# Kernel optimization log

Measured on AMD Instinct MI355X. Metric: run time of the kernel, lower is better.

## Reference

```python
import jax, jax.numpy as jnp
import numpy as np

N_NODES = 50000
N_EDGES = 800000
DIM = 64


def _param(key, shape, scale):
    return jax.random.normal(key, shape, dtype=jnp.float32) * scale


def setup_inputs() -> dict:
    key = jax.random.key(0)
    ks = jax.random.split(key, 20)
    s = 1.0 / np.sqrt(DIM)
    x = jax.random.normal(ks[0], (N_NODES, DIM), dtype=jnp.float32)
    weights = jax.random.uniform(ks[1], (6,), dtype=jnp.float32)
    edge_index = jax.random.randint(ks[2], (2, N_EDGES), 0, N_NODES, dtype=jnp.int64)
    return {
        "x": x,
        "weights": weights,
        # mlp
        "W_mlp": _param(ks[3], (DIM, DIM), s), "b_mlp": jnp.zeros((DIM,), jnp.float32),
        # sage (mean aggregator): lin_l on neighbor mean, lin_r on self
        "Wl_sage": _param(ks[4], (DIM, DIM), s), "Wr_sage": _param(ks[5], (DIM, DIM), s),
        "b_sage": jnp.zeros((DIM,), jnp.float32),
        # gcn
        "W_gcn": _param(ks[6], (DIM, DIM), s), "b_gcn": jnp.zeros((DIM,), jnp.float32),
        # gat (single head)
        "W_gat": _param(ks[7], (DIM, DIM), s),
        "a_src": _param(ks[8], (DIM,), s), "a_dst": _param(ks[9], (DIM,), s),
        "b_gat": jnp.zeros((DIM,), jnp.float32),
        # chebconv K=3
        "W_cheb": _param(ks[10], (3, DIM, DIM), s), "b_cheb": jnp.zeros((DIM,), jnp.float32),
        # gin (eps=0, nn = Linear)
        "W_gin": _param(ks[11], (DIM, DIM), s), "b_gin": jnp.zeros((DIM,), jnp.float32),
        "edge_index": edge_index,
    }


def _mixed_forward(x, weights, W_mlp, b_mlp, Wl_sage, Wr_sage, b_sage,
                   W_gcn, b_gcn, W_gat, a_src, a_dst, b_gat,
                   W_cheb, b_cheb, W_gin, b_gin, edge_index):
    N = x.shape[0]
    src, dst = edge_index[0], edge_index[1]
    seg_sum = lambda v, idx: jax.ops.segment_sum(v, idx, num_segments=N)

    deg = seg_sum(jnp.ones(src.shape[0], x.dtype), dst)  # in-degree [N]
    nsum = seg_sum(x[src], dst)                           # sum of neighbor feats [N, D]

    # --- mlp (graph-free) ---
    o_mlp = x @ W_mlp + b_mlp

    # --- sage, mean aggregation ---
    nmean = nsum / jnp.maximum(deg, 1.0)[:, None]
    o_sage = nmean @ Wl_sage + x @ Wr_sage + b_sage

    # --- gcn with self loops: D'^{-1/2} (A+I) D'^{-1/2} X W ---
    dinv = jax.lax.rsqrt(deg + 1.0)
    xw = x @ W_gcn
    norm_e = dinv[src] * dinv[dst]
    o_gcn = seg_sum(norm_e[:, None] * xw[src], dst) + xw * (dinv * dinv)[:, None] + b_gcn

    # --- gat, single head, self loops appended, leaky_relu(0.2) scoring ---
    h = x @ W_gat
    el, er = h @ a_src, h @ a_dst
    loop = jnp.arange(N, dtype=src.dtype)
    src2 = jnp.concatenate([src, loop])
    dst2 = jnp.concatenate([dst, loop])
    e = jax.nn.leaky_relu(el[src2] + er[dst2], 0.2)
    m = jax.ops.segment_max(e, dst2, num_segments=N)
    p = jnp.exp(e - m[dst2])
    z = jax.ops.segment_sum(p, dst2, num_segments=N)
    alpha = p / (z[dst2] + 1e-16)
    o_gat = jax.ops.segment_sum(alpha[:, None] * h[src2], dst2, num_segments=N) + b_gat

    # --- cheb K=3, lambda_max=2: L_hat = L_norm - I = -A_norm ---
    dinv_c = jax.lax.rsqrt(jnp.maximum(deg, 1.0))
    nrm = dinv_c[src] * dinv_c[dst]
    prop = lambda t: seg_sum(nrm[:, None] * t[src], dst)
    T0 = x
    T1 = -prop(T0)
    T2 = -2.0 * prop(T1) - T0
    o_cheb = T0 @ W_cheb[0] + T1 @ W_cheb[1] + T2 @ W_cheb[2] + b_cheb

    # --- gin, eps=0, nn = Linear ---
    o_gin = (x + nsum) @ W_gin + b_gin

    outs = (o_mlp, o_sage, o_gcn, o_gat, o_cheb, o_gin)
    res = jnp.zeros_like(o_mlp)
    for k, o in enumerate(outs):
        res = res + weights[k] * jax.nn.elu(o)
    return res


def reference(x, weights, W_mlp, b_mlp, Wl_sage, Wr_sage, b_sage,
              W_gcn, b_gcn, W_gat, a_src, a_dst, b_gat,
              W_cheb, b_cheb, W_gin, b_gin, edge_index):
    return _mixed_forward(x, weights, W_mlp, b_mlp, Wl_sage, Wr_sage, b_sage,
                          W_gcn, b_gcn, W_gat, a_src, a_dst, b_gat,
                          W_cheb, b_cheb, W_gin, b_gin, edge_index)
```

## Files before the change

### kernel.cpp

```cpp
#include <hip/hip_runtime.h>
#include <cstdint>
#include <cstddef>

#define NN 50000
#define NE 800000
#define CAP 96

constexpr size_t O_CNT   = 0;
constexpr size_t O_SLOT  = 50048;
constexpr size_t O_NODAL = O_SLOT + (size_t)NN*CAP;
constexpr size_t O_VA    = O_NODAL + 200000;
constexpr size_t O_VB    = O_VA + 64;
constexpr size_t O_XB    = O_VB + 64;
constexpr size_t O_NSB   = O_XB + 1600032;
constexpr size_t O_T1B   = O_NSB + 1600000;
constexpr size_t O_V1B   = O_T1B + 1600032;
constexpr size_t O_GB    = O_V1B + 1600000;
constexpr size_t O_UB    = O_GB  + 1600000;
constexpr size_t O_WPK   = O_UB  + 1600000;

typedef __attribute__((ext_vector_type(8))) short short8;
typedef __attribute__((ext_vector_type(4))) float f32x4;

__device__ __forceinline__ float leaky02(float v){ return v >= 0.f ? v : 0.2f*v; }
__device__ __forceinline__ float eluf(float v){ return v > 0.f ? v : (__expf(v) - 1.f); }

__device__ __forceinline__ void lds_fence(){
  asm volatile("s_waitcnt lgkmcnt(0)" ::: "memory");
}

__device__ __forceinline__ unsigned short f2bf(float f){
  unsigned u = __float_as_uint(f);
  unsigned r = (u + 0x7FFFu + ((u >> 16) & 1u)) >> 16;
  return (unsigned short)r;
}
__device__ __forceinline__ float bf2f(unsigned short b){
  return __uint_as_float(((unsigned)b) << 16);
}

__global__ void k_scatter(const int4* __restrict__ src4, const int4* __restrict__ dst4,
                          int* __restrict__ cnt, int* __restrict__ slot){
  int i = blockIdx.x*256 + threadIdx.x;
  if (i >= NE/4) return;
  int4 s = src4[i], d = dst4[i];
  int pos;
  pos = atomicAdd(&cnt[d.x], 1); if (pos < CAP) slot[(size_t)d.x*CAP + pos] = s.x;
  pos = atomicAdd(&cnt[d.y], 1); if (pos < CAP) slot[(size_t)d.y*CAP + pos] = s.y;
  pos = atomicAdd(&cnt[d.z], 1); if (pos < CAP) slot[(size_t)d.z*CAP + pos] = s.z;
  pos = atomicAdd(&cnt[d.w], 1); if (pos < CAP) slot[(size_t)d.w*CAP + pos] = s.w;
}

__global__ void k_xcast(const float4* __restrict__ x4, ushort4* __restrict__ xb4,
                        ushort4* __restrict__ t1b4){
  int i = blockIdx.x*256 + threadIdx.x;
  if (i < NN*16){
    float4 v = x4[i];
    ushort4 o;
    o.x = f2bf(v.x); o.y = f2bf(v.y); o.z = f2bf(v.z); o.w = f2bf(v.w);
    xb4[i] = o;
  } else if (i < (NN+1)*16){
    ushort4 z; z.x = 0; z.y = 0; z.z = 0; z.w = 0;
    xb4[i] = z;
    t1b4[i] = z;
  }
}

__global__ void k_va(const float* __restrict__ Wg, const float* __restrict__ a_src,
                     const float* __restrict__ a_dst, float* __restrict__ va, float* __restrict__ vb){
  int k = threadIdx.x;
  float sa = 0.f, sb = 0.f;
  for (int j = 0; j < 64; ++j){
    float w = Wg[k*64 + j];
    sa = fmaf(w, a_src[j], sa);
    sb = fmaf(w, a_dst[j], sb);
  }
  va[k] = sa; vb[k] = sb;
}

__global__ void k_wprep(const float* __restrict__ W_mlp, const float* __restrict__ Wr,
                        const float* __restrict__ W_cheb, const float* __restrict__ W_gin,
                        const float* __restrict__ Wl, const float* __restrict__ W_gcn,
                        const float* __restrict__ W_gat, unsigned short* __restrict__ wpk){
  int w = blockIdx.x;
  const float* s; const float* sub = nullptr;
  switch (w){
    case 0: s = W_mlp; break;
    case 1: s = Wr; break;
    case 2: s = W_cheb; sub = W_cheb + 8192; break;
    case 3: s = W_gin; break;
    case 4: s = Wl; break;
    case 5: s = W_cheb + 4096; break;
    case 6: s = W_cheb + 8192; break;
    case 7: s = W_gcn; break;
    default: s = W_gat; break;
  }
  for (int e = threadIdx.x; e < 4096; e += 256){
    int k = e >> 6, n = e & 63;
    float f = s[e];
    if (sub) f -= sub[e];
    wpk[(size_t)w*4096 + (size_t)n*64 + k] = f2bf(f);
  }
}

__global__ __launch_bounds__(256) void k_nodal(const float* __restrict__ x,
    const int* __restrict__ cnt, const float* __restrict__ va, const float* __restrict__ vb,
    float4* __restrict__ nodal){
  int tid = threadIdx.x;
  int li = tid & 15;
  int row = blockIdx.x*16 + (tid >> 4);
  if (row >= NN) return;
  float4 hv = *(const float4*)&x[(size_t)row*64 + li*4];
  float4 av = *(const float4*)&va[li*4];
  float4 bv = *(const float4*)&vb[li*4];
  float ps = hv.x*av.x + hv.y*av.y + hv.z*av.z + hv.w*av.w;
  float pd = hv.x*bv.x + hv.y*bv.y + hv.z*bv.z + hv.w*bv.w;
  #pragma unroll
  for (int o = 1; o < 16; o <<= 1){ ps += __shfl_xor(ps, o); pd += __shfl_xor(pd, o); }
  if (li == 0){
    float c = (float)cnt[row];
    float dinv  = rsqrtf(c + 1.f);
    float dinvc = rsqrtf(fmaxf(c, 1.f));
    nodal[row] = make_float4(dinvc, dinv, ps, pd);
  }
}

__global__ __launch_bounds__(256) void k_aggA(const float* __restrict__ x,
    const unsigned short* __restrict__ xb,
    const int* __restrict__ cnt, const int* __restrict__ slot,
    const float4* __restrict__ nodal,
    unsigned short* __restrict__ nsb, unsigned short* __restrict__ t1b,
    unsigned short* __restrict__ v1b, unsigned short* __restrict__ gb){
  __shared__ float4 sW[4][64];
  int wid  = threadIdx.x >> 6;
  int lane = threadIdx.x & 63;
  int node = blockIdx.x*4 + wid;
  if (node >= NN) return;
  int c = min(cnt[node], CAP);
  const int* sl = slot + (size_t)node*CAP;
  float4 nn = nodal[node];
  float ern = nn.w;
  float a0 = 0.f, a1 = 0.f, a2 = 0.f, a3 = 0.f, zl = 0.f;
  for (int base = 0; base < c; base += 64){
    int rem = min(64, c - base);
    bool act = lane < rem;
    int s = act ? sl[base+lane] : NN;
    float4 ns = act ? nodal[s] : make_float4(0.f,0.f,0.f,0.f);
    float p = act ? __expf(fminf(leaky02(ns.z + ern), 60.f)) : 0.f;
    zl += p;
    sW[wid][lane] = make_float4(__int_as_float(s), ns.x, ns.y, p);
    lds_fence();
    for (int j = 0; j < rem; j += 8){
      float4 w[8];
      #pragma unroll
      for (int jj = 0; jj < 8; ++jj) w[jj] = sW[wid][j + jj];
      float vv[8];
      #pragma unroll
      for (int jj = 0; jj < 8; ++jj){
        int sb = __float_as_int(w[jj].x);
        sb = ((unsigned)sb <= (unsigned)NN) ? sb : NN;
        vv[jj] = bf2f(xb[(size_t)sb*64 + lane]);
      }
      #pragma unroll
      for (int jj = 0; jj < 8; ++jj){
        a0 += vv[jj];
        a1 = fmaf(w[jj].y, vv[jj], a1);
        a2 = fmaf(w[jj].z, vv[jj], a2);
        a3 = fmaf(w[jj].w, vv[jj], a3);
      }
    }
    lds_fence();
  }
  #pragma unroll
  for (int o = 32; o > 0; o >>= 1) zl += __shfl_xor(zl, o);
  float xs = x[(size_t)node*64 + lane];
  float p_self = __expf(fminf(leaky02(nn.z + nn.w), 60.f));
  float rz = 1.f / (zl + p_self + 1e-16f);
  size_t off = (size_t)node*64 + lane;
  nsb[off] = f2bf(a0);
  t1b[off] = f2bf(-nn.x * a1);
  v1b[off] = f2bf(nn.y*a2 + nn.y*nn.y*xs);
  gb[off]  = f2bf((a3 + p_self*xs) * rz);
}

__global__ __launch_bounds__(256) void k_aggB(const unsigned short* __restrict__ t1b,
    const int* __restrict__ cnt, const int* __restrict__ slot,
    const float4* __restrict__ nodal, unsigned short* __restrict__ ub){
  __shared__ float2 sW[4][64];
  int wid  = threadIdx.x >> 6;
  int lane = threadIdx.x & 63;
  int node = blockIdx.x*4 + wid;
  if (node >= NN) return;
  int c = min(cnt[node], CAP);
  const int* sl = slot + (size_t)node*CAP;
  const float* nf = (const float*)nodal;
  float acc = 0.f;
  for (int base = 0; base < c; base += 64){
    int rem = min(64, c - base);
    bool act = lane < rem;
    int s = act ? sl[base+lane] : NN;
    float dc = act ? nf[(size_t)s*4] : 0.f;
    sW[wid][lane] = make_float2(__int_as_float(s), dc);
    lds_fence();
    for (int j = 0; j < rem; j += 8){
      float2 w[8];
      #pragma unroll
      for (int jj = 0; jj < 8; ++jj) w[jj] = sW[wid][j + jj];
      float tv[8];
      #pragma unroll
      for (int jj = 0; jj < 8; ++jj){
        int sb = __float_as_int(w[jj].x);
        sb = ((unsigned)sb <= (unsigned)NN) ? sb : NN;
        tv[jj] = bf2f(t1b[(size_t)sb*64 + lane]);
      }
      #pragma unroll
      for (int jj = 0; jj < 8; ++jj)
        acc = fmaf(w[jj].y, tv[jj], acc);
    }
    lds_fence();
  }
  ub[(size_t)node*64 + lane] = f2bf(-2.f * nodal[node].x * acc);
}

__global__ __launch_bounds__(64) void k_epi(
    const float* __restrict__ wts,
    const float* __restrict__ b_mlp, const float* __restrict__ b_sage,
    const float* __restrict__ b_gcn, const float* __restrict__ b_gat,
    const float* __restrict__ b_cheb, const float* __restrict__ b_gin,
    const float4* __restrict__ nodal, const unsigned short* __restrict__ wpk,
    const unsigned short* __restrict__ xb, const unsigned short* __restrict__ nsb,
    const unsigned short* __restrict__ t1b, const unsigned short* __restrict__ v1b,
    const unsigned short* __restrict__ gb, const unsigned short* __restrict__ ub,
    float* __restrict__ out){
  const int lane = threadIdx.x;
  const int ml   = lane & 15;
  const int q    = lane >> 4;
  const int rowbase = blockIdx.x*16;
  const float w0 = wts[0], w1 = wts[1], w2 = wts[2], w3 = wts[3], w4 = wts[4], w5 = wts[5];
  const float* nod = (const float*)nodal;

  short8 ah0, ah1;

  auto loadA = [&](const unsigned short* __restrict__ src){
    const unsigned short* p = src + (size_t)(rowbase + ml)*64 + q*8;
    ah0 = *(const short8*)p;
    ah1 = *(const short8*)(p + 32);
  };
  auto group = [&](int w, f32x4 acc[4]){
    const unsigned short* base = wpk + (size_t)w*4096;
    #pragma unroll
    for (int nt = 0; nt < 4; ++nt){
      const unsigned short* bp = base + (size_t)(nt*16 + ml)*64;
      short8 b0 = *(const short8*)(bp + q*8);
      short8 b1 = *(const short8*)(bp + 32 + q*8);
      acc[nt] = __builtin_amdgcn_mfma_f32_16x16x32_bf16(ah0, b0, acc[nt], 0, 0, 0);
      acc[nt] = __builtin_amdgcn_mfma_f32_16x16x32_bf16(ah1, b1, acc[nt], 0, 0, 0);
    }
  };

  f32x4 res[4];
  #pragma unroll
  for (int i = 0; i < 4; ++i) res[i] = (f32x4){0.f,0.f,0.f,0.f};

  auto emit = [&](const f32x4 acc[4], const float* __restrict__ bias, float wk){
    #pragma unroll
    for (int nt = 0; nt < 4; ++nt){
      float b = bias[nt*16 + ml];
      #pragma unroll
      for (int r = 0; r < 4; ++r) res[nt][r] += wk * eluf(acc[nt][r] + b);
    }
  };

  f32x4 t[4], accC[4], accWr[4], accG[4];

  loadA(v1b);
  #pragma unroll
  for (int i=0;i<4;++i) t[i] = (f32x4){0.f,0.f,0.f,0.f};
  group(7, t); emit(t, b_gcn, w2);
  loadA(gb);
  #pragma unroll
  for (int i=0;i<4;++i) t[i] = (f32x4){0.f,0.f,0.f,0.f};
  group(8, t); emit(t, b_gat, w3);
  loadA(ub);
  #pragma unroll
  for (int i=0;i<4;++i) accC[i] = (f32x4){0.f,0.f,0.f,0.f};
  group(6, accC);
  loadA(t1b);
  group(5, accC);
  loadA(xb);
  #pragma unroll
  for (int i=0;i<4;++i) t[i] = (f32x4){0.f,0.f,0.f,0.f};
  group(0, t); emit(t, b_mlp, w0);
  #pragma unroll
  for (int i=0;i<4;++i) accWr[i] = (f32x4){0.f,0.f,0.f,0.f};
  group(1, accWr);
  group(2, accC); emit(accC, b_cheb, w4);
  #pragma unroll
  for (int i=0;i<4;++i) accG[i] = (f32x4){0.f,0.f,0.f,0.f};
  group(3, accG);
  loadA(nsb);
  group(3, accG); emit(accG, b_gin, w5);
  #pragma unroll
  for (int i=0;i<4;++i) t[i] = (f32x4){0.f,0.f,0.f,0.f};
  group(4, t);
  #pragma unroll
  for (int nt = 0; nt < 4; ++nt){
    float b = b_sage[nt*16 + ml];
    #pragma unroll
    for (int r = 0; r < 4; ++r){
      int row = rowbase + q*4 + r;
      float dc = nod[(size_t)row*4];
      float invd = dc*dc;
      res[nt][r] += w1 * eluf(invd*t[nt][r] + accWr[nt][r] + b);
    }
  }
  #pragma unroll
  for (int nt = 0; nt < 4; ++nt){
    int col = nt*16 + ml;
    #pragma unroll
    for (int r = 0; r < 4; ++r){
      int row = rowbase + q*4 + r;
      out[(size_t)row*64 + col] = res[nt][r];
    }
  }
}

extern "C" void kernel_launch(void* const* d_in, const int* in_sizes, int n_in,
                              void* d_out, int out_size, void* d_ws, size_t ws_size,
                              hipStream_t stream){
  const float* x      = (const float*)d_in[0];
  const float* wts    = (const float*)d_in[1];
  const float* W_mlp  = (const float*)d_in[2];
  const float* b_mlp  = (const float*)d_in[3];
  const float* Wl     = (const float*)d_in[4];
  const float* Wr     = (const float*)d_in[5];
  const float* b_sage = (const float*)d_in[6];
  const float* W_gcn  = (const float*)d_in[7];
  const float* b_gcn  = (const float*)d_in[8];
  const float* W_gat  = (const float*)d_in[9];
  const float* a_src  = (const float*)d_in[10];
  const float* a_dst  = (const float*)d_in[11];
  const float* b_gat  = (const float*)d_in[12];
  const float* W_cheb = (const float*)d_in[13];
  const float* b_cheb = (const float*)d_in[14];
  const float* W_gin  = (const float*)d_in[15];
  const float* b_gin  = (const float*)d_in[16];
  const int*   ei     = (const int*)d_in[17];

  float* wsf  = (float*)d_ws;
  int*  cnt   = (int*)d_ws;
  int*  slot  = (int*)(wsf + O_SLOT);
  float4* nodal = (float4*)(wsf + O_NODAL);
  float* va   = wsf + O_VA;
  float* vb   = wsf + O_VB;
  unsigned short* xbu = (unsigned short*)(wsf + O_XB);
  unsigned short* nsb = (unsigned short*)(wsf + O_NSB);
  unsigned short* t1b = (unsigned short*)(wsf + O_T1B);
  unsigned short* v1b = (unsigned short*)(wsf + O_V1B);
  unsigned short* gb  = (unsigned short*)(wsf + O_GB);
  unsigned short* ub  = (unsigned short*)(wsf + O_UB);
  unsigned short* wpk = (unsigned short*)(wsf + O_WPK);
  float* out  = (float*)d_out;

  hipMemsetAsync(cnt, 0, NN*sizeof(int), stream);
  k_scatter <<<782,  256, 0, stream>>>((const int4*)ei, (const int4*)(ei + NE), cnt, slot);
  k_va      <<<1,     64, 0, stream>>>(W_gat, a_src, a_dst, va, vb);
  k_wprep   <<<9,    256, 0, stream>>>(W_mlp, Wr, W_cheb, W_gin, Wl, W_gcn, W_gat, wpk);
  k_xcast   <<<3126, 256, 0, stream>>>((const float4*)x, (ushort4*)xbu, (ushort4*)t1b);
  k_nodal   <<<3125, 256, 0, stream>>>(x, cnt, va, vb, nodal);
  k_aggA    <<<12500,256, 0, stream>>>(x, xbu, cnt, slot, nodal, nsb, t1b, v1b, gb);
  k_aggB    <<<12500,256, 0, stream>>>(t1b, cnt, slot, nodal, ub);
  k_epi     <<<3125,  64, 0, stream>>>(wts, b_mlp, b_sage, b_gcn, b_gat, b_cheb, b_gin,
                                       nodal, wpk, xbu, nsb, t1b, v1b, gb, ub, out);
}
```

Baseline: 242.9 us.

## Use 16-bit neighbor slots, half-wave paired bf16 gathers, and merge prep kernels

```diff
diff --git a/kernel.cpp b/kernel.cpp
--- a/kernel.cpp
+++ b/kernel.cpp
@@ -37,22 +37,65 @@
 __device__ __forceinline__ float bf2f(unsigned short b){
   return __uint_as_float(((unsigned)b) << 16);
 }
-
-__global__ void k_scatter(const int4* __restrict__ src4, const int4* __restrict__ dst4,
-                          int* __restrict__ cnt, int* __restrict__ slot){
-  int i = blockIdx.x*256 + threadIdx.x;
-  if (i >= NE/4) return;
-  int4 s = src4[i], d = dst4[i];
-  int pos;
-  pos = atomicAdd(&cnt[d.x], 1); if (pos < CAP) slot[(size_t)d.x*CAP + pos] = s.x;
-  pos = atomicAdd(&cnt[d.y], 1); if (pos < CAP) slot[(size_t)d.y*CAP + pos] = s.y;
-  pos = atomicAdd(&cnt[d.z], 1); if (pos < CAP) slot[(size_t)d.z*CAP + pos] = s.z;
-  pos = atomicAdd(&cnt[d.w], 1); if (pos < CAP) slot[(size_t)d.w*CAP + pos] = s.w;
-}
-
-__global__ void k_xcast(const float4* __restrict__ x4, ushort4* __restrict__ xb4,
-                        ushort4* __restrict__ t1b4){
-  int i = blockIdx.x*256 + threadIdx.x;
+__device__ __forceinline__ unsigned pack2(unsigned short lo, unsigned short hi){
+  return (unsigned)lo | ((unsigned)hi << 16);
+}
+
+__global__ void k_scatter(const int* __restrict__ src, const int* __restrict__ dst,
+                          int* __restrict__ cnt, unsigned short* __restrict__ slot){
+  int e = blockIdx.x*256 + threadIdx.x;
+  if (e >= NE) return;
+  int s = src[e], d = dst[e];
+  int pos = atomicAdd(&cnt[d], 1);
+  if (pos < CAP) slot[(size_t)d*CAP + pos] = (unsigned short)s;
+}
+
+__global__ void k_prep(const float* __restrict__ W_mlp, const float* __restrict__ Wr,
+                       const float* __restrict__ W_cheb, const float* __restrict__ W_gin,
+                       const float* __restrict__ Wl, const float* __restrict__ W_gcn,
+                       const float* __restrict__ W_gat,
+                       const float* __restrict__ a_src, const float* __restrict__ a_dst,
+                       const float4* __restrict__ x4,
+                       float* __restrict__ va, float* __restrict__ vb,
+                       unsigned short* __restrict__ wpk,
+                       ushort4* __restrict__ xb4, ushort4* __restrict__ t1b4){
+  int b = blockIdx.x;
+  if (b == 0){
+    int k = threadIdx.x;
+    if (k < 64){
+      float sa = 0.f, sb = 0.f;
+      for (int j = 0; j < 64; ++j){
+        float w = W_gat[k*64 + j];
+        sa = fmaf(w, a_src[j], sa);
+        sb = fmaf(w, a_dst[j], sb);
+      }
+      va[k] = sa; vb[k] = sb;
+    }
+    return;
+  }
+  if (b <= 9){
+    int w = b - 1;
+    const float* s; const float* sub = nullptr;
+    switch (w){
+      case 0: s = W_mlp; break;
+      case 1: s = Wr; break;
+      case 2: s = W_cheb; sub = W_cheb + 8192; break;
+      case 3: s = W_gin; break;
+      case 4: s = Wl; break;
+      case 5: s = W_cheb + 4096; break;
+      case 6: s = W_cheb + 8192; break;
+      case 7: s = W_gcn; break;
+      default: s = W_gat; break;
+    }
+    for (int e = threadIdx.x; e < 4096; e += 256){
+      int k = e >> 6, n = e & 63;
+      float f = s[e];
+      if (sub) f -= sub[e];
+      wpk[(size_t)w*4096 + (size_t)n*64 + k] = f2bf(f);
+    }
+    return;
+  }
+  int i = (b - 10)*256 + threadIdx.x;
   if (i < NN*16){
     float4 v = x4[i];
     ushort4 o;
@@ -62,43 +105,6 @@
     ushort4 z; z.x = 0; z.y = 0; z.z = 0; z.w = 0;
     xb4[i] = z;
     t1b4[i] = z;
-  }
-}
-
-__global__ void k_va(const float* __restrict__ Wg, const float* __restrict__ a_src,
-                     const float* __restrict__ a_dst, float* __restrict__ va, float* __restrict__ vb){
-  int k = threadIdx.x;
-  float sa = 0.f, sb = 0.f;
-  for (int j = 0; j < 64; ++j){
-    float w = Wg[k*64 + j];
-    sa = fmaf(w, a_src[j], sa);
-    sb = fmaf(w, a_dst[j], sb);
-  }
-  va[k] = sa; vb[k] = sb;
-}
-
-__global__ void k_wprep(const float* __restrict__ W_mlp, const float* __restrict__ Wr,
-                        const float* __restrict__ W_cheb, const float* __restrict__ W_gin,
-                        const float* __restrict__ Wl, const float* __restrict__ W_gcn,
-                        const float* __restrict__ W_gat, unsigned short* __restrict__ wpk){
-  int w = blockIdx.x;
-  const float* s; const float* sub = nullptr;
-  switch (w){
-    case 0: s = W_mlp; break;
-    case 1: s = Wr; break;
-    case 2: s = W_cheb; sub = W_cheb + 8192; break;
-    case 3: s = W_gin; break;
-    case 4: s = Wl; break;
-    case 5: s = W_cheb + 4096; break;
-    case 6: s = W_cheb + 8192; break;
-    case 7: s = W_gcn; break;
-    default: s = W_gat; break;
-  }
-  for (int e = threadIdx.x; e < 4096; e += 256){
-    int k = e >> 6, n = e & 63;
-    float f = s[e];
-    if (sub) f -= sub[e];
-    wpk[(size_t)w*4096 + (size_t)n*64 + k] = f2bf(f);
   }
 }
 
@@ -126,99 +132,115 @@
 
 __global__ __launch_bounds__(256) void k_aggA(const float* __restrict__ x,
     const unsigned short* __restrict__ xb,
-    const int* __restrict__ cnt, const int* __restrict__ slot,
+    const int* __restrict__ cnt, const unsigned short* __restrict__ slot,
     const float4* __restrict__ nodal,
-    unsigned short* __restrict__ nsb, unsigned short* __restrict__ t1b,
-    unsigned short* __restrict__ v1b, unsigned short* __restrict__ gb){
+    unsigned* __restrict__ nsb2, unsigned* __restrict__ t1b2,
+    unsigned* __restrict__ v1b2, unsigned* __restrict__ gb2){
   __shared__ float4 sW[4][64];
   int wid  = threadIdx.x >> 6;
   int lane = threadIdx.x & 63;
   int node = blockIdx.x*4 + wid;
   if (node >= NN) return;
   int c = min(cnt[node], CAP);
-  const int* sl = slot + (size_t)node*CAP;
+  const unsigned short* sl = slot + (size_t)node*CAP;
   float4 nn = nodal[node];
   float ern = nn.w;
-  float a0 = 0.f, a1 = 0.f, a2 = 0.f, a3 = 0.f, zl = 0.f;
+  int half = lane >> 5, hl = lane & 31;
+  float a0e=0.f,a0o=0.f,a1e=0.f,a1o=0.f,a2e=0.f,a2o=0.f,a3e=0.f,a3o=0.f, zl=0.f;
   for (int base = 0; base < c; base += 64){
     int rem = min(64, c - base);
     bool act = lane < rem;
-    int s = act ? sl[base+lane] : NN;
+    int s = act ? (int)sl[base+lane] : NN;
     float4 ns = act ? nodal[s] : make_float4(0.f,0.f,0.f,0.f);
     float p = act ? __expf(fminf(leaky02(ns.z + ern), 60.f)) : 0.f;
     zl += p;
     sW[wid][lane] = make_float4(__int_as_float(s), ns.x, ns.y, p);
     lds_fence();
     for (int j = 0; j < rem; j += 8){
-      float4 w[8];
-      #pragma unroll
-      for (int jj = 0; jj < 8; ++jj) w[jj] = sW[wid][j + jj];
-      float vv[8];
-      #pragma unroll
-      for (int jj = 0; jj < 8; ++jj){
-        int sb = __float_as_int(w[jj].x);
+      float4 w[4]; unsigned uv[4];
+      #pragma unroll
+      for (int q2 = 0; q2 < 4; ++q2){
+        w[q2] = sW[wid][j + 2*q2 + half];
+        int sb = __float_as_int(w[q2].x);
         sb = ((unsigned)sb <= (unsigned)NN) ? sb : NN;
-        vv[jj] = bf2f(xb[(size_t)sb*64 + lane]);
-      }
-      #pragma unroll
-      for (int jj = 0; jj < 8; ++jj){
-        a0 += vv[jj];
-        a1 = fmaf(w[jj].y, vv[jj], a1);
-        a2 = fmaf(w[jj].z, vv[jj], a2);
-        a3 = fmaf(w[jj].w, vv[jj], a3);
+        uv[q2] = *(const unsigned*)&xb[(size_t)sb*64 + 2*hl];
+      }
+      #pragma unroll
+      for (int q2 = 0; q2 < 4; ++q2){
+        float lo = __uint_as_float(uv[q2] << 16);
+        float hi = __uint_as_float(uv[q2] & 0xffff0000u);
+        a0e += lo;                       a0o += hi;
+        a1e = fmaf(w[q2].y, lo, a1e);    a1o = fmaf(w[q2].y, hi, a1o);
+        a2e = fmaf(w[q2].z, lo, a2e);    a2o = fmaf(w[q2].z, hi, a2o);
+        a3e = fmaf(w[q2].w, lo, a3e);    a3o = fmaf(w[q2].w, hi, a3o);
       }
     }
     lds_fence();
   }
+  a0e += __shfl_xor(a0e, 32); a0o += __shfl_xor(a0o, 32);
+  a1e += __shfl_xor(a1e, 32); a1o += __shfl_xor(a1o, 32);
+  a2e += __shfl_xor(a2e, 32); a2o += __shfl_xor(a2o, 32);
+  a3e += __shfl_xor(a3e, 32); a3o += __shfl_xor(a3o, 32);
   #pragma unroll
   for (int o = 32; o > 0; o >>= 1) zl += __shfl_xor(zl, o);
-  float xs = x[(size_t)node*64 + lane];
+  float2 xs = *(const float2*)&x[(size_t)node*64 + 2*hl];
   float p_self = __expf(fminf(leaky02(nn.z + nn.w), 60.f));
   float rz = 1.f / (zl + p_self + 1e-16f);
-  size_t off = (size_t)node*64 + lane;
-  nsb[off] = f2bf(a0);
-  t1b[off] = f2bf(-nn.x * a1);
-  v1b[off] = f2bf(nn.y*a2 + nn.y*nn.y*xs);
-  gb[off]  = f2bf((a3 + p_self*xs) * rz);
+  size_t off2 = (size_t)node*32 + hl;
+  if (half == 0){
+    nsb2[off2] = pack2(f2bf(a0e), f2bf(a0o));
+    t1b2[off2] = pack2(f2bf(-nn.x*a1e), f2bf(-nn.x*a1o));
+  } else {
+    v1b2[off2] = pack2(f2bf(nn.y*a2e + nn.y*nn.y*xs.x), f2bf(nn.y*a2o + nn.y*nn.y*xs.y));
+    gb2[off2]  = pack2(f2bf((a3e + p_self*xs.x)*rz), f2bf((a3o + p_self*xs.y)*rz));
+  }
 }
 
 __global__ __launch_bounds__(256) void k_aggB(const unsigned short* __restrict__ t1b,
-    const int* __restrict__ cnt, const int* __restrict__ slot,
-    const float4* __restrict__ nodal, unsigned short* __restrict__ ub){
+    const int* __restrict__ cnt, const unsigned short* __restrict__ slot,
+    const float4* __restrict__ nodal, unsigned* __restrict__ ub2){
   __shared__ float2 sW[4][64];
   int wid  = threadIdx.x >> 6;
   int lane = threadIdx.x & 63;
   int node = blockIdx.x*4 + wid;
   if (node >= NN) return;
   int c = min(cnt[node], CAP);
-  const int* sl = slot + (size_t)node*CAP;
+  const unsigned short* sl = slot + (size_t)node*CAP;
   const float* nf = (const float*)nodal;
-  float acc = 0.f;
+  int half = lane >> 5, hl = lane & 31;
+  float ae = 0.f, ao = 0.f;
   for (int base = 0; base < c; base += 64){
     int rem = min(64, c - base);
     bool act = lane < rem;
-    int s = act ? sl[base+lane] : NN;
+    int s = act ? (int)sl[base+lane] : NN;
     float dc = act ? nf[(size_t)s*4] : 0.f;
     sW[wid][lane] = make_float2(__int_as_float(s), dc);
     lds_fence();
     for (int j = 0; j < rem; j += 8){
-      float2 w[8];
-      #pragma unroll
-      for (int jj = 0; jj < 8; ++jj) w[jj] = sW[wid][j + jj];
-      float tv[8];
-      #pragma unroll
-      for (int jj = 0; jj < 8; ++jj){
-        int sb = __float_as_int(w[jj].x);
+      float2 w[4]; unsigned uv[4];
+      #pragma unroll
+      for (int q2 = 0; q2 < 4; ++q2){
+        w[q2] = sW[wid][j + 2*q2 + half];
+        int sb = __float_as_int(w[q2].x);
         sb = ((unsigned)sb <= (unsigned)NN) ? sb : NN;
-        tv[jj] = bf2f(t1b[(size_t)sb*64 + lane]);
-      }
-      #pragma unroll
-      for (int jj = 0; jj < 8; ++jj)
-        acc = fmaf(w[jj].y, tv[jj], acc);
+        uv[q2] = *(const unsigned*)&t1b[(size_t)sb*64 + 2*hl];
+      }
+      #pragma unroll
+      for (int q2 = 0; q2 < 4; ++q2){
+        float lo = __uint_as_float(uv[q2] << 16);
+        float hi = __uint_as_float(uv[q2] & 0xffff0000u);
+        ae = fmaf(w[q2].y, lo, ae);
+        ao = fmaf(w[q2].y, hi, ao);
+      }
     }
     lds_fence();
   }
-  ub[(size_t)node*64 + lane] = f2bf(-2.f * nodal[node].x * acc);
+  ae += __shfl_xor(ae, 32);
+  ao += __shfl_xor(ao, 32);
+  if (half == 0){
+    float sc = -2.f * nodal[node].x;
+    ub2[(size_t)node*32 + hl] = pack2(f2bf(sc*ae), f2bf(sc*ao));
+  }
 }
 
 __global__ __launch_bounds__(64) void k_epi(
@@ -348,7 +370,7 @@
 
   float* wsf  = (float*)d_ws;
   int*  cnt   = (int*)d_ws;
-  int*  slot  = (int*)(wsf + O_SLOT);
+  unsigned short* slot = (unsigned short*)(wsf + O_SLOT);
   float4* nodal = (float4*)(wsf + O_NODAL);
   float* va   = wsf + O_VA;
   float* vb   = wsf + O_VB;
@@ -362,13 +384,15 @@
   float* out  = (float*)d_out;
 
   hipMemsetAsync(cnt, 0, NN*sizeof(int), stream);
-  k_scatter <<<782,  256, 0, stream>>>((const int4*)ei, (const int4*)(ei + NE), cnt, slot);
-  k_va      <<<1,     64, 0, stream>>>(W_gat, a_src, a_dst, va, vb);
-  k_wprep   <<<9,    256, 0, stream>>>(W_mlp, Wr, W_cheb, W_gin, Wl, W_gcn, W_gat, wpk);
-  k_xcast   <<<3126, 256, 0, stream>>>((const float4*)x, (ushort4*)xbu, (ushort4*)t1b);
+  k_scatter <<<3125, 256, 0, stream>>>(ei, ei + NE, cnt, slot);
+  k_prep    <<<3136, 256, 0, stream>>>(W_mlp, Wr, W_cheb, W_gin, Wl, W_gcn, W_gat,
+                                       a_src, a_dst, (const float4*)x,
+                                       va, vb, wpk, (ushort4*)xbu, (ushort4*)t1b);
   k_nodal   <<<3125, 256, 0, stream>>>(x, cnt, va, vb, nodal);
-  k_aggA    <<<12500,256, 0, stream>>>(x, xbu, cnt, slot, nodal, nsb, t1b, v1b, gb);
-  k_aggB    <<<12500,256, 0, stream>>>(t1b, cnt, slot, nodal, ub);
+  k_aggA    <<<12500,256, 0, stream>>>(x, xbu, cnt, slot, nodal,
+                                       (unsigned*)nsb, (unsigned*)t1b,
+                                       (unsigned*)v1b, (unsigned*)gb);
+  k_aggB    <<<12500,256, 0, stream>>>(t1b, cnt, slot, nodal, (unsigned*)ub);
   k_epi     <<<3125,  64, 0, stream>>>(wts, b_mlp, b_sage, b_gcn, b_gat, b_cheb, b_gin,
                                        nodal, wpk, xbu, nsb, t1b, v1b, gb, ub, out);
 }
```

Measured after the change: 241.7 us. About the same (-0.5%).
